# Kernel tuning notes

Hardware: AMD Instinct MI355X
Metric: run time of the kernel (lower is better)

Reference implementation:

```python
import jax, jax.numpy as jnp
import numpy as np

N_HEAD = 16
D_QK = 128
D_V = 128
D_MODEL = 2048
BATCH = 2
SEQ = 2048


def alibi_slopes(n_head):
    # standard ALiBi slopes: 2^(-8*i/n_head) for i = 1..n_head
    return jnp.asarray(2.0 ** (-8.0 * np.arange(1, n_head + 1) / n_head), dtype=jnp.float32)


def setup_inputs() -> dict:
    key = jax.random.key(0)
    k1, k2, k3, k4, k5 = jax.random.split(key, 5)
    x = jax.random.normal(k1, (BATCH, SEQ, D_MODEL), dtype=jnp.float32)
    # causal attention mask (1 = keep, 0 = masked), broadcast over heads
    causal = jnp.tril(jnp.ones((SEQ, SEQ), dtype=bool))
    attention_mask = jnp.broadcast_to(causal, (BATCH, 1, SEQ, SEQ))
    Wq = jax.random.normal(k2, (D_MODEL, N_HEAD * D_QK), dtype=jnp.float32) * (D_MODEL ** -0.5)
    Wk = jax.random.normal(k3, (D_MODEL, N_HEAD * D_QK), dtype=jnp.float32) * (D_MODEL ** -0.5)
    Wv = jax.random.normal(k4, (D_MODEL, N_HEAD * D_V), dtype=jnp.float32) * (D_MODEL ** -0.5)
    Wo = jax.random.normal(k5, (N_HEAD * D_V, D_MODEL), dtype=jnp.float32) * ((N_HEAD * D_V) ** -0.5)
    return {"x": x, "attention_mask": attention_mask, "Wq": Wq, "Wk": Wk, "Wv": Wv, "Wo": Wo}


def reference(x, attention_mask, Wq, Wk, Wv, Wo):
    B, S, _ = x.shape
    scale = D_QK ** -0.5
    q = (x @ Wq).reshape(B, S, N_HEAD, D_QK).transpose(0, 2, 1, 3)  # [B,H,S,dqk]
    k = (x @ Wk).reshape(B, S, N_HEAD, D_QK).transpose(0, 2, 1, 3)
    v = (x @ Wv).reshape(B, S, N_HEAD, D_V).transpose(0, 2, 1, 3)
    scores = jnp.einsum('bhid,bhjd->bhij', q, k) * scale  # [B,H,S,S]
    # ALiBi bias: slope_h * (j - i), negative penalty for distant past keys
    pos = jnp.arange(S, dtype=jnp.float32)
    rel = pos[None, :] - pos[:, None]  # [S,S]
    slopes = alibi_slopes(N_HEAD)
    scores = scores + slopes[None, :, None, None] * rel[None, None, :, :]
    scores = jnp.where(attention_mask, scores, jnp.float32(-jnp.inf))
    attn = jax.nn.softmax(scores, axis=-1)
    out = jnp.einsum('bhij,bhjd->bhid', attn, v)  # [B,H,S,dv]
    out = out.transpose(0, 2, 1, 3).reshape(B, S, N_HEAD * D_V)
    return out @ Wo
```

## Files before the change

kernel.cpp:

```cpp
#include <hip/hip_runtime.h>
#include <cstdint>

typedef unsigned short u16;
typedef __attribute__((ext_vector_type(4))) u16 u16x4;
typedef __attribute__((ext_vector_type(8))) u16 u16x8;
typedef __attribute__((ext_vector_type(8))) __bf16 bf16x8;
typedef __attribute__((ext_vector_type(4))) float f32x4;

#define LOG2E 1.44269504088896340736f

static __device__ __forceinline__ u16 f2bf(float f) {
  unsigned u = __builtin_bit_cast(unsigned, f);
  u += 0x7fffu + ((u >> 16) & 1u);
  return (u16)(u >> 16);
}
static __device__ __forceinline__ float bf2f(u16 v) {
  unsigned u = ((unsigned)v) << 16;
  return __builtin_bit_cast(float, u);
}

static __device__ __forceinline__ void gload16(const u16* g, u16* l) {
  __builtin_amdgcn_global_load_lds(
      (__attribute__((address_space(1))) void*)(uintptr_t)g,
      (__attribute__((address_space(3))) void*)(uintptr_t)l, 16, 0, 0);
}

static __device__ __forceinline__ bf16x8 lds_bf8(const void* p) {
  return __builtin_bit_cast(bf16x8, *(const u16x8*)p);
}

__global__ __launch_bounds__(256) void cast_x_kernel(const float* __restrict__ src,
                                                     u16* __restrict__ dst) {
  int i = (blockIdx.x * 256 + threadIdx.x) * 4;
  float4 v = *(const float4*)(src + i);
  u16x4 r = {f2bf(v.x), f2bf(v.y), f2bf(v.z), f2bf(v.w)};
  *(u16x4*)(dst + i) = r;
}

__device__ __forceinline__ void transpose_body(const float* __restrict__ src,
                                               u16* __restrict__ dst) {
  __shared__ float tile[32][33];
  const int n0 = blockIdx.x * 32, k0 = blockIdx.y * 32;
  const int tx = threadIdx.x & 31, ty = threadIdx.x >> 5;
#pragma unroll
  for (int r = 0; r < 4; ++r) {
    int row = r * 8 + ty;
    tile[row][tx] = src[(size_t)(k0 + row) * 2048 + n0 + tx];
  }
  __syncthreads();
#pragma unroll
  for (int r = 0; r < 4; ++r) {
    int row = r * 8 + ty;
    dst[(size_t)(n0 + row) * 2048 + k0 + tx] = f2bf(tile[tx][row]);
  }
}

__global__ __launch_bounds__(256) void transpose_w_kernel(const float* __restrict__ src,
                                                          u16* __restrict__ dst) {
  transpose_body(src, dst);
}

__global__ __launch_bounds__(256) void transpose_w3_kernel(const float* Wq, const float* Wk,
                                                           const float* Wv, u16* Wqt, u16* Wkt,
                                                           u16* Wvt) {
  const float* src = blockIdx.z == 0 ? Wq : (blockIdx.z == 1 ? Wk : Wv);
  u16* dst = blockIdx.z == 0 ? Wqt : (blockIdx.z == 1 ? Wkt : Wvt);
  transpose_body(src, dst);
}

#define GSTAGE(TILE, KH, BUF)                                                        \
  do {                                                                               \
    const int bk = (TILE) * 64 + (KH) * 32;                                          \
    u16* as_ = &lds[((BUF) * 2 + (KH)) * 8192];                                      \
    u16* bs_ = &lds[32768 + ((BUF) * 2 + (KH)) * BSLOT];                             \
    gload16(&A[(size_t)(m0 + sr) * 2048 + bk + scu], as_ + tid * 8);                 \
    gload16(&A[(size_t)(m0 + 128 + sr) * 2048 + bk + scu], as_ + 4096 + tid * 8);    \
    gload16(&Bt[(size_t)(n0 + sr) * 2048 + bk + scu], bs_ + tid * 8);                \
    if constexpr (BN == 256)                                                         \
      gload16(&Bt[(size_t)(n0 + 128 + sr) * 2048 + bk + scu], bs_ + 4096 + tid * 8); \
  } while (0)

#define GPH(BUF, KH, STAGE_STMT, VMLIT)                                              \
  do {                                                                               \
    const u16* as_ = &lds[((BUF) * 2 + (KH)) * 8192];                                \
    const u16* bs_ = &lds[32768 + ((BUF) * 2 + (KH)) * BSLOT];                       \
    bf16x8 af[8], bq[NF];                                                            \
    _Pragma("unroll") for (int mf = 0; mf < 8; ++mf) {                               \
      const int ar = wm * 128 + mf * 16 + l16;                                       \
      af[mf] = lds_bf8(&as_[(ar * 32 + lg * 8) ^ xsw]);                              \
    }                                                                                \
    _Pragma("unroll") for (int nf = 0; nf < NF; ++nf) {                              \
      const int br = wn * (BN / 4) + nf * 16 + l16;                                  \
      bq[nf] = lds_bf8(&bs_[(br * 32 + lg * 8) ^ xsw]);                              \
    }                                                                                \
    STAGE_STMT;                                                                      \
    asm volatile("s_barrier" ::: "memory");                                          \
    __builtin_amdgcn_s_setprio(1);                                                   \
    _Pragma("unroll") for (int mf = 0; mf < 8; ++mf)                                 \
        _Pragma("unroll") for (int nf = 0; nf < NF; ++nf) acc[mf][nf] =              \
            __builtin_amdgcn_mfma_f32_16x16x32_bf16(af[mf], bq[nf], acc[mf][nf], 0, 0, 0); \
    __builtin_amdgcn_s_setprio(0);                                                   \
    __builtin_amdgcn_sched_barrier(0);                                               \
    asm volatile("s_waitcnt vmcnt(" #VMLIT ")\n\ts_barrier" ::: "memory");           \
  } while (0)

template <int BN, int MODE>
__device__ __forceinline__ void gemm_dp(const u16* __restrict__ A, const u16* __restrict__ Bt,
                                        void* __restrict__ Cout, int m0, int n0) {
  constexpr int BSLOT = BN * 32;
  constexpr int NF = BN / 64;
  __shared__ u16 lds[32768 + 4 * BSLOT];
  const int tid = threadIdx.x, lane = tid & 63, w = tid >> 6;
  const int wm = w >> 2, wn = w & 3;
  const int l16 = lane & 15, lg = lane >> 4;
  const int sr = tid >> 2;
  const int scu = (((tid & 3) ^ ((tid >> 2) & 3))) * 8;
  const int xsw = (l16 & 3) * 8;

  f32x4 acc[8][NF];
#pragma unroll
  for (int i = 0; i < 8; ++i)
#pragma unroll
    for (int j = 0; j < NF; ++j) acc[i][j] = f32x4{0.f, 0.f, 0.f, 0.f};

  GSTAGE(0, 0, 0);
  GSTAGE(0, 1, 0);
  GSTAGE(1, 0, 1);
  if constexpr (BN == 256) {
    asm volatile("s_waitcnt vmcnt(8)\n\ts_barrier" ::: "memory");
    for (int m2 = 0; m2 < 30; m2 += 2) {
      GPH(0, 0, GSTAGE(m2 + 1, 1, 1), 8);
      GPH(0, 1, GSTAGE(m2 + 2, 0, 0), 8);
      GPH(1, 0, GSTAGE(m2 + 2, 1, 0), 8);
      GPH(1, 1, GSTAGE(m2 + 3, 0, 1), 8);
    }
    GPH(0, 0, GSTAGE(31, 1, 1), 8);
    GPH(0, 1, (void)0, 4);
    GPH(1, 0, (void)0, 0);
    GPH(1, 1, (void)0, 0);
  } else {
    asm volatile("s_waitcnt vmcnt(6)\n\ts_barrier" ::: "memory");
    for (int m2 = 0; m2 < 30; m2 += 2) {
      GPH(0, 0, GSTAGE(m2 + 1, 1, 1), 6);
      GPH(0, 1, GSTAGE(m2 + 2, 0, 0), 6);
      GPH(1, 0, GSTAGE(m2 + 2, 1, 0), 6);
      GPH(1, 1, GSTAGE(m2 + 3, 0, 1), 6);
    }
    GPH(0, 0, GSTAGE(31, 1, 1), 6);
    GPH(0, 1, (void)0, 3);
    GPH(1, 0, (void)0, 0);
    GPH(1, 1, (void)0, 0);
  }

  constexpr int WNS = BN / 4;
#pragma unroll
  for (int mf = 0; mf < 8; ++mf)
#pragma unroll
    for (int nf = 0; nf < NF; ++nf)
#pragma unroll
      for (int r = 0; r < 4; ++r) {
        const int row = m0 + wm * 128 + mf * 16 + lg * 4 + r;
        const int col = n0 + wn * WNS + nf * 16 + l16;
        const float v = acc[mf][nf][r];
        if constexpr (MODE == 0) {
          size_t off =
              (((size_t)(row >> 11) * 16 + (col >> 7)) * 2048 + (row & 2047)) * 128 + (col & 127);
          ((u16*)Cout)[off] = f2bf(v);
        } else if constexpr (MODE == 2) {
          size_t off =
              (((size_t)(col >> 11) * 16 + (row >> 7)) * 128 + (row & 127)) * 2048 + (col & 2047);
          ((u16*)Cout)[off] = f2bf(v);
        } else {
          ((float*)Cout)[(size_t)row * 2048 + col] = v;
        }
      }
}

__global__ __launch_bounds__(512, 2) void qkproj_kernel(const u16* xb, const u16* Wqt,
                                                        const u16* Wkt, u16* Qb, u16* Kb) {
  const int n0g = blockIdx.y * 256;
  const u16* Bt = (n0g < 2048) ? Wqt : Wkt;
  u16* dst = (n0g < 2048) ? Qb : Kb;
  gemm_dp<256, 0>(xb, Bt, dst, blockIdx.x * 256, n0g & 2047);
}

__global__ __launch_bounds__(512, 2) void vt_kernel(const u16* Wvt, const u16* xb, u16* Vb) {
  gemm_dp<128, 2>(Wvt, xb, Vb, blockIdx.x * 256, blockIdx.y * 128);
}

__global__ __launch_bounds__(512, 2) void out_kernel(const u16* OA, const u16* Wot, float* C) {
  gemm_dp<128, 1>(OA, Wot, C, blockIdx.x * 256, blockIdx.y * 128);
}

__global__ __launch_bounds__(256) void attn_kernel(const u16* __restrict__ Q,
                                                   const u16* __restrict__ Kg,
                                                   const u16* __restrict__ Vg,
                                                   u16* __restrict__ O,
                                                   u16* __restrict__ Opart,
                                                   float* __restrict__ Lp) {
  const int tid = threadIdx.x, lane = tid & 63, w = tid >> 6;
  const int l16 = lane & 15, lg = lane >> 4;

  const int bid = blockIdx.x;
  const int bh = bid / 23, u = bid - bh * 23;
  int tile, st0, st1, slot = 0;
  bool multi;
  if (u < 14) {
    multi = true;
    const int ti = u >> 1, ch = u & 1;
    tile = 9 + ti;
    const int s = 2 * tile + 2;
    st0 = ch * 18;
    st1 = min(st0 + 18, s);
    slot = bh * 14 + u;
  } else {
    multi = false;
    tile = 22 - u;
    st0 = 0;
    st1 = 2 * tile + 2;
  }
  const int q0 = tile * 128;
  const int h = bh & 15, b = bh >> 4;
  const float sl2 = exp2f(-0.5f * (float)(h + 1)) * LOG2E;
  const float sc2 = 0.08838834764831845f * LOG2E;

  __shared__ u16 Kl[2][64 * 128];
  __shared__ u16 Vl[2][128 * 64];
  __shared__ u16 Pl[128 * 64];

  const size_t qk_base = (size_t)bh * 2048 * 128;
  const size_t v_base = (size_t)bh * 128 * 2048;

  bf16x8 qf[2][4];
#pragma unroll
  for (int mf = 0; mf < 2; ++mf)
#pragma unroll
    for (int ks = 0; ks < 4; ++ks)
      qf[mf][ks] =
          lds_bf8(&Q[qk_base + (size_t)(q0 + w * 32 + mf * 16 + l16) * 128 + ks * 32 + lg * 8]);

  f32x4 oacc[2][8];
#pragma unroll
  for (int i = 0; i < 2; ++i)
#pragma unroll
    for (int j = 0; j < 8; ++j) oacc[i][j] = f32x4{0.f, 0.f, 0.f, 0.f};
  float lsum[2][2];
  lsum[0][0] = lsum[0][1] = lsum[1][0] = lsum[1][1] = 0.f;

  float ab[2][4][4];
#pragma unroll
  for (int mf = 0; mf < 2; ++mf)
#pragma unroll
    for (int nf = 0; nf < 4; ++nf)
#pragma unroll
      for (int r = 0; r < 4; ++r)
        ab[mf][nf][r] =
            (float)(st0 * 64 + nf * 16 + lg * 4 + r - q0 - w * 32 - mf * 16 - l16) * sl2;
  const float abinc = 64.0f * sl2;

  const u16* kgp = Kg + qk_base + (size_t)(tid >> 4) * 128 + (tid & 15) * 8;
  const u16* vgp = Vg + v_base + (size_t)(tid >> 3) * 2048 + (tid & 7) * 8;
  const int kwo = ((tid >> 4) * 256 + (tid & 15) * 16) ^ (((tid >> 4) & 7) << 4);
  const int vwo = ((tid >> 3) * 128 + (tid & 7) * 16) ^ (((tid >> 3) & 7) << 4);

  u16x8 kr[4], vr[4];
#define LOADREGS(STX)                                                        \
  do {                                                                       \
    const size_t ko = (size_t)(STX)*8192, vo = (size_t)(STX)*64;             \
    _Pragma("unroll") for (int s = 0; s < 4; ++s) {                          \
      kr[s] = *(const u16x8*)(kgp + ko + s * 2048);                          \
      vr[s] = *(const u16x8*)(vgp + vo + s * 65536);                         \
    }                                                                        \
  } while (0)

#define WRITEBUF(BI)                                                         \
  do {                                                                       \
    _Pragma("unroll") for (int s = 0; s < 4; ++s) {                          \
      *(u16x8*)((char*)Kl[BI] + s * 4096 + kwo) = kr[s];                     \
      *(u16x8*)((char*)Vl[BI] + s * 4096 + vwo) = vr[s];                     \
    }                                                                        \
  } while (0)

#define ASTEP(MASKED)                                                                     \
  do {                                                                                    \
    if (st + 1 < st1) WRITEBUF(cur ^ 1);                                                  \
    if (st + 2 < st1) LOADREGS(st + 2);                                                   \
    f32x4 sacc[2][4];                                                                     \
    _Pragma("unroll") for (int i = 0; i < 2; ++i)                                         \
        _Pragma("unroll") for (int j = 0; j < 4; ++j) sacc[i][j] = f32x4{0.f, 0.f, 0.f, 0.f}; \
    __builtin_amdgcn_s_setprio(1);                                                        \
    _Pragma("unroll") for (int ks = 0; ks < 4; ++ks) {                                    \
      bf16x8 kf[4];                                                                       \
      _Pragma("unroll") for (int nf = 0; nf < 4; ++nf) {                                  \
        int j = nf * 16 + l16;                                                            \
        kf[nf] = lds_bf8((char*)Kl[cur] + ((j * 256 + (ks * 32 + lg * 8) * 2) ^ ((j & 7) << 4))); \
      }                                                                                   \
      _Pragma("unroll") for (int mf = 0; mf < 2; ++mf)                                    \
          _Pragma("unroll") for (int nf = 0; nf < 4; ++nf) sacc[mf][nf] =                 \
              __builtin_amdgcn_mfma_f32_16x16x32_bf16(kf[nf], qf[mf][ks], sacc[mf][nf], 0, 0, 0); \
    }                                                                                     \
    __builtin_amdgcn_s_setprio(0);                                                        \
    _Pragma("unroll") for (int mf = 0; mf < 2; ++mf)                                      \
        _Pragma("unroll") for (int nf = 0; nf < 4; ++nf) {                                \
      u16x4 pw;                                                                           \
      float pvv[4];                                                                       \
      _Pragma("unroll") for (int r = 0; r < 4; ++r) {                                     \
        float s2 = fmaf(sacc[mf][nf][r], sc2, ab[mf][nf][r]);                             \
        float pv = exp2f(s2);                                                             \
        if (MASKED) {                                                                     \
          const int rel = st * 64 + nf * 16 + lg * 4 + r - q0 - w * 32 - mf * 16 - l16;   \
          pv = (rel <= 0) ? pv : 0.f;                                                     \
        }                                                                                 \
        pvv[r] = pv;                                                                      \
        pw[r] = f2bf(pv);                                                                 \
        ab[mf][nf][r] += abinc;                                                           \
      }                                                                                   \
      lsum[mf][nf & 1] += (pvv[0] + pvv[1]) + (pvv[2] + pvv[3]);                          \
      const int qrow = w * 32 + mf * 16 + l16;                                            \
      *(u16x4*)((char*)Pl + ((qrow * 128 + (nf * 16 + lg * 4) * 2) ^ ((qrow & 7) << 4))) = pw; \
    }                                                                                     \
    __builtin_amdgcn_s_setprio(1);                                                        \
    _Pragma("unroll") for (int ks = 0; ks < 2; ++ks) {                                    \
      bf16x8 pf[2];                                                                       \
      _Pragma("unroll") for (int mf = 0; mf < 2; ++mf) {                                  \
        int qrow = w * 32 + mf * 16 + l16;                                                \
        pf[mf] = lds_bf8((char*)Pl + ((qrow * 128 + (ks * 32 + lg * 8) * 2) ^ ((qrow & 7) << 4))); \
      }                                                                                   \
      _Pragma("unroll") for (int nf = 0; nf < 8; ++nf) {                                  \
        int d = nf * 16 + l16;                                                            \
        bf16x8 vf =                                                                       \
            lds_bf8((char*)Vl[cur] + ((d * 128 + (ks * 32 + lg * 8) * 2) ^ ((d & 7) << 4))); \
        _Pragma("unroll") for (int mf = 0; mf < 2; ++mf) oacc[mf][nf] =                   \
            __builtin_amdgcn_mfma_f32_16x16x32_bf16(pf[mf], vf, oacc[mf][nf], 0, 0, 0);   \
      }                                                                                   \
    }                                                                                     \
    __builtin_amdgcn_s_setprio(0);                                                        \
    __syncthreads();                                                                      \
    cur ^= 1;                                                                             \
  } while (0)

  LOADREGS(st0);
  WRITEBUF(0);
  if (st0 + 1 < st1) LOADREGS(st0 + 1);
  __syncthreads();

  int cur = 0;
  const int dstart = (multi && (u & 1) == 0) ? st1 : st1 - 2;
  int st = st0;
  for (; st < dstart; ++st) ASTEP(false);
  for (; st < st1; ++st) ASTEP(true);
#undef LOADREGS
#undef WRITEBUF
#undef ASTEP

  float lr[2];
#pragma unroll
  for (int mf = 0; mf < 2; ++mf) {
    float v = lsum[mf][0] + lsum[mf][1];
    v += __shfl_xor(v, 16, 64);
    v += __shfl_xor(v, 32, 64);
    lr[mf] = v;
  }

  if (multi) {
    if (lg == 0) {
#pragma unroll
      for (int mf = 0; mf < 2; ++mf) Lp[(size_t)slot * 128 + w * 32 + mf * 16 + l16] = lr[mf];
    }
#pragma unroll
    for (int mf = 0; mf < 2; ++mf)
#pragma unroll
      for (int r = 0; r < 4; ++r) {
        const int row = w * 32 + mf * 16 + lg * 4 + r;
#pragma unroll
        for (int nf = 0; nf < 8; ++nf) {
          int col = nf * 16 + l16;
          Opart[((size_t)slot * 128 + row) * 128 + col] = f2bf(oacc[mf][nf][r]);
        }
      }
  } else {
#pragma unroll
    for (int mf = 0; mf < 2; ++mf)
#pragma unroll
      for (int r = 0; r < 4; ++r) {
        const float lv = __shfl(lr[mf], lg * 4 + r, 64);
        const float inv = 1.0f / lv;
        const int srow = q0 + w * 32 + mf * 16 + lg * 4 + r;
#pragma unroll
        for (int nf = 0; nf < 8; ++nf) {
          int col = h * 128 + nf * 16 + l16;
          O[((size_t)b * 2048 + srow) * 2048 + col] = f2bf(oacc[mf][nf][r] * inv);
        }
      }
  }
}

__global__ __launch_bounds__(256) void combine_kernel(const u16* __restrict__ Opart,
                                                      const float* __restrict__ Lp,
                                                      u16* __restrict__ O) {
  const int bx = blockIdx.x;
  const int bh = bx / 7, ti = bx % 7;
  const int tile = 9 + ti;
  const int slot0 = bh * 14 + ti * 2, slot1 = slot0 + 1;
  const int b = bh >> 4, h = bh & 15;
  const int q0 = tile * 128;
  const int tid = threadIdx.x;
  const int colg = (tid & 15) * 8, rowb = tid >> 4;
#pragma unroll
  for (int rr = 0; rr < 8; ++rr) {
    const int row = rowb + rr * 16;
    const float l0 = Lp[(size_t)slot0 * 128 + row];
    const float l1 = Lp[(size_t)slot1 * 128 + row];
    const float inv = 1.0f / (l0 + l1);
    u16x8 p0 = *(const u16x8*)&Opart[((size_t)slot0 * 128 + row) * 128 + colg];
    u16x8 p1 = *(const u16x8*)&Opart[((size_t)slot1 * 128 + row) * 128 + colg];
    u16x8 o;
#pragma unroll
    for (int e = 0; e < 8; ++e) o[e] = f2bf((bf2f(p0[e]) + bf2f(p1[e])) * inv);
    *(u16x8*)&O[((size_t)b * 2048 + q0 + row) * 2048 + h * 128 + colg] = o;
  }
}

extern "C" void kernel_launch(void* const* d_in, const int* in_sizes, int n_in, void* d_out,
                              int out_size, void* d_ws, size_t ws_size, hipStream_t stream) {
  const float* x = (const float*)d_in[0];
  const float* Wq = (const float*)d_in[2];
  const float* Wk = (const float*)d_in[3];
  const float* Wv = (const float*)d_in[4];
  const float* Wo = (const float*)d_in[5];
  char* ws = (char*)d_ws;

  const size_t MB = 1048576;
  u16* xb = (u16*)(ws);
  u16* Qb = (u16*)(ws + 16 * MB);
  u16* Kb = (u16*)(ws + 32 * MB);
  u16* Vb = (u16*)(ws + 48 * MB);
  u16* Wqt = (u16*)(ws + 64 * MB);
  u16* Wkt = (u16*)(ws + 72 * MB);
  u16* Wvt = (u16*)(ws + 80 * MB);
  u16* Wot = Wqt;
  u16* OA = xb;
  u16* Opart = (u16*)(ws + 72 * MB);
  float* Lpf = (float*)(ws + 72 * MB + 448ull * 128 * 128 * 2);

  cast_x_kernel<<<8192, 256, 0, stream>>>(x, xb);
  transpose_w3_kernel<<<dim3(64, 64, 3), 256, 0, stream>>>(Wq, Wk, Wv, Wqt, Wkt, Wvt);
  qkproj_kernel<<<dim3(16, 16), 512, 0, stream>>>(xb, Wqt, Wkt, Qb, Kb);
  vt_kernel<<<dim3(8, 32), 512, 0, stream>>>(Wvt, xb, Vb);
  transpose_w_kernel<<<dim3(64, 64), 256, 0, stream>>>(Wo, Wot);
  attn_kernel<<<dim3(736), 256, 0, stream>>>(Qb, Kb, Vb, OA, Opart, Lpf);
  combine_kernel<<<dim3(224), 256, 0, stream>>>(Opart, Lpf, OA);
  out_kernel<<<dim3(16, 16), 512, 0, stream>>>(OA, Wot, (float*)d_out);
}
```

Before: 283.5 us.

## Single-buffer K/V LDS in attention to fit three blocks per CU

Attention K/V shared tiles go from double to single buffering, cutting LDS per block from 80KB to 48KB, and launch bounds now request 3 blocks per CU. The global prefetch distance drops from two steps to one, and the buffer write now sits between two barriers at the end of each step. P conversion to bf16 uses the packed v_cvt_pk_bf16_f32 instruction. Higher occupancy is meant to hide latency, at the cost of an extra barrier per step, less overlap within a block and tighter register limits.

```diff
diff --git a/kernel.cpp b/kernel.cpp
--- a/kernel.cpp
+++ b/kernel.cpp
@@ -192,12 +192,12 @@
   gemm_dp<128, 1>(OA, Wot, C, blockIdx.x * 256, blockIdx.y * 128);
 }
 
-__global__ __launch_bounds__(256) void attn_kernel(const u16* __restrict__ Q,
-                                                   const u16* __restrict__ Kg,
-                                                   const u16* __restrict__ Vg,
-                                                   u16* __restrict__ O,
-                                                   u16* __restrict__ Opart,
-                                                   float* __restrict__ Lp) {
+__global__ __launch_bounds__(256, 3) void attn_kernel(const u16* __restrict__ Q,
+                                                      const u16* __restrict__ Kg,
+                                                      const u16* __restrict__ Vg,
+                                                      u16* __restrict__ O,
+                                                      u16* __restrict__ Opart,
+                                                      float* __restrict__ Lp) {
   const int tid = threadIdx.x, lane = tid & 63, w = tid >> 6;
   const int l16 = lane & 15, lg = lane >> 4;
 
@@ -224,8 +224,8 @@
   const float sl2 = exp2f(-0.5f * (float)(h + 1)) * LOG2E;
   const float sc2 = 0.08838834764831845f * LOG2E;
 
-  __shared__ u16 Kl[2][64 * 128];
-  __shared__ u16 Vl[2][128 * 64];
+  __shared__ u16 Kl[64 * 128];
+  __shared__ u16 Vl[128 * 64];
   __shared__ u16 Pl[128 * 64];
 
   const size_t qk_base = (size_t)bh * 2048 * 128;
@@ -273,18 +273,17 @@
     }                                                                        \
   } while (0)
 
-#define WRITEBUF(BI)                                                         \
+#define WRITEBUF()                                                           \
   do {                                                                       \
     _Pragma("unroll") for (int s = 0; s < 4; ++s) {                          \
-      *(u16x8*)((char*)Kl[BI] + s * 4096 + kwo) = kr[s];                     \
-      *(u16x8*)((char*)Vl[BI] + s * 4096 + vwo) = vr[s];                     \
+      *(u16x8*)((char*)Kl + s * 4096 + kwo) = kr[s];                         \
+      *(u16x8*)((char*)Vl + s * 4096 + vwo) = vr[s];                         \
     }                                                                        \
   } while (0)
 
 #define ASTEP(MASKED)                                                                     \
   do {                                                                                    \
-    if (st + 1 < st1) WRITEBUF(cur ^ 1);                                                  \
-    if (st + 2 < st1) LOADREGS(st + 2);                                                   \
+    if (st + 1 < st1) LOADREGS(st + 1);                                                   \
     f32x4 sacc[2][4];                                                                     \
     _Pragma("unroll") for (int i = 0; i < 2; ++i)                                         \
         _Pragma("unroll") for (int j = 0; j < 4; ++j) sacc[i][j] = f32x4{0.f, 0.f, 0.f, 0.f}; \
@@ -293,7 +292,7 @@
       bf16x8 kf[4];                                                                       \
       _Pragma("unroll") for (int nf = 0; nf < 4; ++nf) {                                  \
         int j = nf * 16 + l16;                                                            \
-        kf[nf] = lds_bf8((char*)Kl[cur] + ((j * 256 + (ks * 32 + lg * 8) * 2) ^ ((j & 7) << 4))); \
+        kf[nf] = lds_bf8((char*)Kl + ((j * 256 + (ks * 32 + lg * 8) * 2) ^ ((j & 7) << 4))); \
       }                                                                                   \
       _Pragma("unroll") for (int mf = 0; mf < 2; ++mf)                                    \
           _Pragma("unroll") for (int nf = 0; nf < 4; ++nf) sacc[mf][nf] =                 \
@@ -302,7 +301,6 @@
     __builtin_amdgcn_s_setprio(0);                                                        \
     _Pragma("unroll") for (int mf = 0; mf < 2; ++mf)                                      \
         _Pragma("unroll") for (int nf = 0; nf < 4; ++nf) {                                \
-      u16x4 pw;                                                                           \
       float pvv[4];                                                                       \
       _Pragma("unroll") for (int r = 0; r < 4; ++r) {                                     \
         float s2 = fmaf(sacc[mf][nf][r], sc2, ab[mf][nf][r]);                             \
@@ -312,12 +310,15 @@
           pv = (rel <= 0) ? pv : 0.f;                                                     \
         }                                                                                 \
         pvv[r] = pv;                                                                      \
-        pw[r] = f2bf(pv);                                                                 \
         ab[mf][nf][r] += abinc;                                                           \
       }                                                                                   \
       lsum[mf][nf & 1] += (pvv[0] + pvv[1]) + (pvv[2] + pvv[3]);                          \
+      unsigned w0_, w1_;                                                                  \
+      asm("v_cvt_pk_bf16_f32 %0, %1, %2" : "=v"(w0_) : "v"(pvv[0]), "v"(pvv[1]));         \
+      asm("v_cvt_pk_bf16_f32 %0, %1, %2" : "=v"(w1_) : "v"(pvv[2]), "v"(pvv[3]));         \
       const int qrow = w * 32 + mf * 16 + l16;                                            \
-      *(u16x4*)((char*)Pl + ((qrow * 128 + (nf * 16 + lg * 4) * 2) ^ ((qrow & 7) << 4))) = pw; \
+      uint2 pw_{w0_, w1_};                                                                \
+      *(uint2*)((char*)Pl + ((qrow * 128 + (nf * 16 + lg * 4) * 2) ^ ((qrow & 7) << 4))) = pw_; \
     }                                                                                     \
     __builtin_amdgcn_s_setprio(1);                                                        \
     _Pragma("unroll") for (int ks = 0; ks < 2; ++ks) {                                    \
@@ -329,22 +330,23 @@
       _Pragma("unroll") for (int nf = 0; nf < 8; ++nf) {                                  \
         int d = nf * 16 + l16;                                                            \
         bf16x8 vf =                                                                       \
-            lds_bf8((char*)Vl[cur] + ((d * 128 + (ks * 32 + lg * 8) * 2) ^ ((d & 7) << 4))); \
+            lds_bf8((char*)Vl + ((d * 128 + (ks * 32 + lg * 8) * 2) ^ ((d & 7) << 4)));   \
         _Pragma("unroll") for (int mf = 0; mf < 2; ++mf) oacc[mf][nf] =                   \
             __builtin_amdgcn_mfma_f32_16x16x32_bf16(pf[mf], vf, oacc[mf][nf], 0, 0, 0);   \
       }                                                                                   \
     }                                                                                     \
     __builtin_amdgcn_s_setprio(0);                                                        \
-    __syncthreads();                                                                      \
-    cur ^= 1;                                                                             \
+    if (st + 1 < st1) {                                                                   \
+      __syncthreads();                                                                    \
+      WRITEBUF();                                                                         \
+      __syncthreads();                                                                    \
+    }                                                                                     \
   } while (0)
 
   LOADREGS(st0);
-  WRITEBUF(0);
-  if (st0 + 1 < st1) LOADREGS(st0 + 1);
+  WRITEBUF();
   __syncthreads();
 
-  int cur = 0;
   const int dstart = (multi && (u & 1) == 0) ? st1 : st1 - 2;
   int st = st0;
   for (; st < dstart; ++st) ASTEP(false);
```

After: 602.1 us. 2.12x slower.
